# Performance work log

Measured on AMD Instinct MI355X. Metric: run time of the kernel, lower is better.

The kernel has to match this reference:

```python
import jax, jax.numpy as jnp
import numpy as np

N = 20000      # nodes per graph
E = 320000     # edges per graph (before self-loops)
G = 256        # graphs (strings) per side
VOCAB = 128    # NUMBER_EMBEDDINGS
D_IN = 128
HID = 64
H = 4
D_OUT = 128
NEG_SLOPE = 0.2  # PyG GATConv leaky_relu slope


def _gat(x, edge_index, W, att_s, att_d, bias, concat):
    """PyG GATConv: gather -> per-edge logits -> segment softmax over dst -> scatter.
    x: [N, F_in], W: [F_in, H*C], att_s/att_d: [H, C], bias: [H*C] or [C].
    Self-loops are added (PyG default add_self_loops=True)."""
    n = x.shape[0]
    h, c = att_s.shape
    loops = jnp.arange(n)
    src = jnp.concatenate([edge_index[0], loops])  # message sources j
    dst = jnp.concatenate([edge_index[1], loops])  # message targets i
    xh = (x @ W).reshape(n, h, c)                  # [N,H,C]
    a_s = jnp.einsum('nhc,hc->nh', xh, att_s)      # [N,H]
    a_d = jnp.einsum('nhc,hc->nh', xh, att_d)
    logits = jax.nn.leaky_relu(a_s[src] + a_d[dst], NEG_SLOPE)  # [E',H]
    m = jax.ops.segment_max(logits, dst, num_segments=n)
    m = jnp.where(jnp.isfinite(m), m, 0.0)
    e = jnp.exp(logits - m[dst])
    z = jax.ops.segment_sum(e, dst, num_segments=n)
    alpha = e / (z[dst] + 1e-16)                   # [E',H]
    msg = xh[src] * alpha[:, :, None]              # [E',H,C]
    out = jax.ops.segment_sum(msg, dst, num_segments=n)  # [N,H,C]
    out = out.reshape(n, h * c) if concat else out.mean(axis=1)
    return out + bias


def _encode(xi, ei, batch, emb, W1, as1, ad1, b1, lw1, lb1,
            W2, as2, ad2, b2, lw2, lb2, W3, as3, ad3, b3, lw3, lb3):
    e = emb[xi]  # [N, D_IN]
    x = jax.nn.relu(_gat(e, ei, W1, as1, ad1, b1, True) + e @ lw1 + lb1)
    x = jax.nn.relu(_gat(x, ei, W2, as2, ad2, b2, True) + x @ lw2 + lb2)
    x = _gat(x, ei, W3, as3, ad3, b3, False) + x @ lw3 + lb3  # [N, D_OUT]
    s = jax.ops.segment_sum(x, batch, num_segments=G)
    cnt = jax.ops.segment_sum(jnp.ones((x.shape[0],), x.dtype), batch, num_segments=G)
    return s / jnp.maximum(cnt, 1.0)[:, None]  # global_mean_pool -> [G, D_OUT]


def setup_inputs() -> dict:
    key = jax.random.key(0)
    ks = jax.random.split(key, 32)
    hc = H * HID  # 256
    def nrm(k, shape, scale=0.05):
        return jax.random.normal(k, shape, dtype=jnp.float32) * scale
    inp = {
        'x_l': jax.random.randint(ks[0], (N,), 0, VOCAB),
        'edge_l': jax.random.randint(ks[1], (2, E), 0, N),
        'batch_l': jnp.sort(jax.random.randint(ks[2], (N,), 0, G)),
        'x_r': jax.random.randint(ks[3], (N,), 0, VOCAB),
        'edge_r': jax.random.randint(ks[4], (2, E), 0, N),
        'batch_r': jnp.sort(jax.random.randint(ks[5], (N,), 0, G)),
        'emb': nrm(ks[6], (VOCAB, D_IN), 1.0),
        'W1': nrm(ks[7], (D_IN, hc)), 'as1': nrm(ks[8], (H, HID)), 'ad1': nrm(ks[9], (H, HID)),
        'b1': jnp.zeros((hc,), jnp.float32), 'lw1': nrm(ks[10], (D_IN, hc)), 'lb1': jnp.zeros((hc,), jnp.float32),
        'W2': nrm(ks[11], (hc, hc)), 'as2': nrm(ks[12], (H, HID)), 'ad2': nrm(ks[13], (H, HID)),
        'b2': jnp.zeros((hc,), jnp.float32), 'lw2': nrm(ks[14], (hc, hc)), 'lb2': jnp.zeros((hc,), jnp.float32),
        'W3': nrm(ks[15], (hc, H * D_OUT)), 'as3': nrm(ks[16], (H, D_OUT)), 'ad3': nrm(ks[17], (H, D_OUT)),
        'b3': jnp.zeros((D_OUT,), jnp.float32), 'lw3': nrm(ks[18], (hc, D_OUT)), 'lb3': jnp.zeros((D_OUT,), jnp.float32),
    }
    return inp


def reference(x_l, edge_l, batch_l, x_r, edge_r, batch_r, emb,
              W1, as1, ad1, b1, lw1, lb1,
              W2, as2, ad2, b2, lw2, lb2,
              W3, as3, ad3, b3, lw3, lb3):
    params = (emb, W1, as1, ad1, b1, lw1, lb1, W2, as2, ad2, b2, lw2, lb2,
              W3, as3, ad3, b3, lw3, lb3)
    out_l = _encode(x_l, edge_l, batch_l, *params)
    out_r = _encode(x_r, edge_r, batch_r, *params)
    return (out_l, out_r)
```

## Files before the change

kernel.cpp:

```cpp
#include <hip/hip_runtime.h>

#define GG 256

typedef __bf16 bf16x8 __attribute__((ext_vector_type(8)));
typedef __bf16 bf16x4 __attribute__((ext_vector_type(4)));
typedef float floatx4 __attribute__((ext_vector_type(4)));
typedef float f32x2 __attribute__((ext_vector_type(2)));

__device__ __forceinline__ float lrelu(float x) { return x > 0.f ? x : 0.2f * x; }

__device__ __forceinline__ int permM(int m) {
    int g = m >> 6, q = m & 63;
    return (g << 6) | ((q & 3) << 4) | (q >> 2);
}

__device__ __forceinline__ void wt1(const float* __restrict__ B, __bf16* __restrict__ Bt,
                                    int K, int M, int idx) {
    int k = idx / M, m = idx - k * M;
    Bt[(size_t)permM(m) * K + k] = (__bf16)B[idx];
}
__device__ __forceinline__ void wattn1(const float* __restrict__ W,
                                       const float* __restrict__ as_,
                                       const float* __restrict__ ad_,
                                       __bf16* __restrict__ dst, int K, int C, int idx) {
    int j = idx / K, k = idx - j * K;
    float v = 0.f;
    if (j < 8) {
        int h = j & 3;
        const float* att = (j < 4) ? as_ : ad_;
        int M = 4 * C;
        for (int c = 0; c < C; c++) v += W[(size_t)k * M + h * C + c] * att[h * C + c];
    }
    dst[(size_t)j * K + k] = (__bf16)v;
}

__global__ void k_wprep(const float* W1, const float* lw1, const float* as1, const float* ad1,
                        const float* W2, const float* lw2, const float* as2, const float* ad2,
                        const float* W3, const float* lw3, const float* as3, const float* ad3,
                        __bf16* B1t, __bf16* B2t, __bf16* B3t) {
    int idx = blockIdx.x * blockDim.x + threadIdx.x;
    if (idx < 32768) { wt1(W1, B1t, 128, 256, idx); return; }
    idx -= 32768;
    if (idx < 32768) { wt1(lw1, B1t + 256 * 128, 128, 256, idx); return; }
    idx -= 32768;
    if (idx < 2048) { wattn1(W1, as1, ad1, B1t + 512 * 128, 128, 64, idx); return; }
    idx -= 2048;
    if (idx < 65536) { wt1(W2, B2t, 256, 256, idx); return; }
    idx -= 65536;
    if (idx < 65536) { wt1(lw2, B2t + 256 * 256, 256, 256, idx); return; }
    idx -= 65536;
    if (idx < 4096) { wattn1(W2, as2, ad2, B2t + 512 * 256, 256, 64, idx); return; }
    idx -= 4096;
    if (idx < 131072) { wt1(W3, B3t, 256, 512, idx); return; }
    idx -= 131072;
    if (idx < 32768) { wt1(lw3, B3t + 512 * 256, 256, 128, idx); return; }
    idx -= 32768;
    if (idx < 4096) { wattn1(W3, as3, ad3, B3t + 640 * 256, 256, 128, idx); return; }
}

template <int K, bool EMB, bool LINBF>
__global__ __launch_bounds__(256) void k_gemm_all(const __bf16* __restrict__ A,
                                                  const int* __restrict__ xl,
                                                  const int* __restrict__ xr,
                                                  const float* __restrict__ emb,
                                                  const __bf16* __restrict__ Bt,
                                                  int n, int n1, int Mx, int Ml,
                                                  unsigned char* __restrict__ x8, int ldx,
                                                  float* __restrict__ linf,
                                                  __bf16* __restrict__ linb, int ldl,
                                                  const float* __restrict__ bias1,
                                                  const float* __restrict__ bias2,
                                                  float* __restrict__ a_s,
                                                  float* __restrict__ a_d) {
    constexpr int KS = K / 32;
    constexpr int LDK = K + 8;
    constexpr int LPR = K / 8;
    constexpr int NCH = 64 * LPR / 256;
    __shared__ __bf16 S[64 * LDK];
    int tid = threadIdx.x;
    int wave = tid >> 6, lane = tid & 63;
    int row0 = blockIdx.x * 64;
#pragma unroll
    for (int c = 0; c < NCH; c++) {
        int i = tid + c * 256;
        int r = i / LPR, ko = (i - r * LPR) * 8;
        int gr = row0 + r;
        bf16x8 v = {};
        if (gr < n) {
            if (EMB) {
                int xi = (gr < n1) ? xl[gr] : xr[gr - n1];
                const float4* src = (const float4*)(emb + ((size_t)xi << 7) + ko);
                float4 q0 = src[0], q1 = src[1];
                v = bf16x8{(__bf16)q0.x, (__bf16)q0.y, (__bf16)q0.z, (__bf16)q0.w,
                           (__bf16)q1.x, (__bf16)q1.y, (__bf16)q1.z, (__bf16)q1.w};
            } else {
                v = *(const bf16x8*)(A + (size_t)gr * K + ko);
            }
        }
        *(bf16x8*)&S[r * LDK + ko] = v;
    }
    __syncthreads();
    int kOff = (lane >> 4) * 8;
    int colBase = lane & 15;
    bf16x8 af[KS];
#pragma unroll
    for (int ks = 0; ks < KS; ks++)
        af[ks] = *(const bf16x8*)&S[(wave * 16 + colBase) * LDK + ks * 32 + kOff];
    int Mtot = Mx + Ml;
    int gr0 = row0 + wave * 16 + ((lane >> 4) << 2);
    int half = (Mtot / 128) * 64;
    int c0beg = blockIdx.y * half;
    int T = half / 64;
    bf16x8 regs[NCH];
#pragma unroll
    for (int c = 0; c < NCH; c++) {
        int i = tid + c * 256;
        int r = i / LPR, ko = (i - r * LPR) * 8;
        regs[c] = *(const bf16x8*)(Bt + (size_t)(c0beg + r) * K + ko);
    }
    for (int t = 0; t < T; t++) {
        __syncthreads();
#pragma unroll
        for (int c = 0; c < NCH; c++) {
            int i = tid + c * 256;
            int r = i / LPR, ko = (i - r * LPR) * 8;
            *(bf16x8*)&S[r * LDK + ko] = regs[c];
        }
        if (t + 1 < T) {
            int c0n = c0beg + (t + 1) * 64;
#pragma unroll
            for (int c = 0; c < NCH; c++) {
                int i = tid + c * 256;
                int r = i / LPR, ko = (i - r * LPR) * 8;
                regs[c] = *(const bf16x8*)(Bt + (size_t)(c0n + r) * K + ko);
            }
        }
        __syncthreads();
        floatx4 acc[4] = {};
#pragma unroll
        for (int ct = 0; ct < 4; ct++) {
#pragma unroll
            for (int ks = 0; ks < KS; ks++) {
                bf16x8 bf = *(const bf16x8*)&S[(ct * 16 + colBase) * LDK + ks * 32 + kOff];
                acc[ct] = __builtin_amdgcn_mfma_f32_16x16x32_bf16(af[ks], bf, acc[ct], 0, 0, 0);
            }
        }
        int c0 = c0beg + t * 64;
        if (c0 < Mx) {
#pragma unroll
            for (int r = 0; r < 4; r++) {
                int gr = gr0 + r;
                if (gr >= n) continue;
                int p = __builtin_amdgcn_cvt_pk_fp8_f32(acc[0][r], acc[1][r], 0, false);
                p = __builtin_amdgcn_cvt_pk_fp8_f32(acc[2][r], acc[3][r], p, true);
                *(unsigned int*)(x8 + (size_t)gr * ldx + c0 + colBase * 4) = (unsigned int)p;
            }
        } else {
            int c2 = c0 + colBase * 4 - Mx;
#pragma unroll
            for (int r = 0; r < 4; r++) {
                int gr = gr0 + r;
                if (gr >= n) continue;
                float v0 = acc[0][r] + bias1[c2 + 0];
                float v1 = acc[1][r] + bias1[c2 + 1];
                float v2 = acc[2][r] + bias1[c2 + 2];
                float v3 = acc[3][r] + bias1[c2 + 3];
                if (bias2) {
                    v0 += bias2[c2 + 0]; v1 += bias2[c2 + 1];
                    v2 += bias2[c2 + 2]; v3 += bias2[c2 + 3];
                }
                if (LINBF) {
                    bf16x4 o = {(__bf16)v0, (__bf16)v1, (__bf16)v2, (__bf16)v3};
                    *(bf16x4*)(linb + (size_t)gr * ldl + c2) = o;
                } else {
                    float4 o = {v0, v1, v2, v3};
                    *(float4*)(linf + (size_t)gr * ldl + c2) = o;
                }
            }
        }
    }
    if (blockIdx.y == 1) {
        floatx4 acc = {};
        const __bf16* bp = Bt + (size_t)(Mtot + colBase) * K + kOff;
#pragma unroll
        for (int ks = 0; ks < KS; ks++) {
            bf16x8 bf = *(const bf16x8*)(bp + ks * 32);
            acc = __builtin_amdgcn_mfma_f32_16x16x32_bf16(af[ks], bf, acc, 0, 0, 0);
        }
        if (colBase < 8) {
            float* dst = (colBase < 4) ? a_s : a_d;
            int h = colBase & 3;
#pragma unroll
            for (int r = 0; r < 4; r++) {
                int gr = gr0 + r;
                if (gr < n) dst[gr * 4 + h] = acc[r];
            }
        }
    }
}

__global__ void k_hist2(const int* __restrict__ el, const int* __restrict__ er,
                        int E, int n, int* __restrict__ deg) {
    int e = blockIdx.x * blockDim.x + threadIdx.x;
    if (e >= 2 * E) return;
    int d = (e < E) ? el[E + e] : er[E + (e - E)] + n;
    atomicAdd(&deg[d], 1);
}

__global__ __launch_bounds__(1024) void k_scan1(int* __restrict__ rp, int n,
                                                int* __restrict__ part) {
    __shared__ int wsum[16];
    int i = blockIdx.x * 1024 + threadIdx.x;
    int lane = threadIdx.x & 63, wid = threadIdx.x >> 6;
    int v = (i < n) ? rp[i] : 0;
    int inc = v;
#pragma unroll
    for (int off = 1; off < 64; off <<= 1) {
        int t = __shfl_up(inc, off, 64);
        if (lane >= off) inc += t;
    }
    if (lane == 63) wsum[wid] = inc;
    __syncthreads();
    if (wid == 0) {
        int wv = (lane < 16) ? wsum[lane] : 0;
        int winc = wv;
#pragma unroll
        for (int off = 1; off < 16; off <<= 1) {
            int t = __shfl_up(winc, off, 64);
            if (lane >= off) winc += t;
        }
        if (lane < 16) wsum[lane] = winc - wv;
        if (lane == 15) part[blockIdx.x] = winc;
    }
    __syncthreads();
    if (i < n) rp[i] = wsum[wid] + (inc - v);
}

__global__ void k_scan2(int* __restrict__ part, int nb) {
    int lane = threadIdx.x;
    int v = (lane < nb) ? part[lane] : 0;
    int inc = v;
#pragma unroll
    for (int off = 1; off < 64; off <<= 1) {
        int t = __shfl_up(inc, off, 64);
        if (lane >= off) inc += t;
    }
    if (lane < nb) part[lane] = inc - v;
}

__global__ __launch_bounds__(1024) void k_scan3(int* __restrict__ rp, int n,
                                                const int* __restrict__ part) {
    int i = blockIdx.x * 1024 + threadIdx.x;
    if (i < n) rp[i] += part[blockIdx.x];
}

__global__ void k_fill2(const int* __restrict__ el, const int* __restrict__ er,
                        int E, int n, int* __restrict__ rp, int* __restrict__ csr) {
    int e = blockIdx.x * blockDim.x + threadIdx.x;
    if (e >= 2 * E) return;
    int d, s;
    if (e < E) { s = el[e]; d = el[E + e]; }
    else       { s = er[e - E] + n; d = er[E + (e - E)] + n; }
    int pos = atomicAdd(&rp[d], 1);
    csr[pos] = s;
}

__device__ __forceinline__ void dec4(unsigned int u, float* f) {
    f32x2 a = __builtin_amdgcn_cvt_pk_f32_fp8(u, false);
    f32x2 b = __builtin_amdgcn_cvt_pk_f32_fp8(u, true);
    f[0] = a[0]; f[1] = a[1]; f[2] = b[0]; f[3] = b[1];
}

__global__ __launch_bounds__(256) void k_agg12(const int* __restrict__ rp,
                                               const int* __restrict__ csr,
                                               const float* __restrict__ a_s,
                                               const float* __restrict__ a_d,
                                               const unsigned char* __restrict__ x8,
                                               const __bf16* __restrict__ lin,
                                               __bf16* __restrict__ out_bf, int n) {
    int wv = (int)((blockIdx.x * blockDim.x + threadIdx.x) >> 6);
    int lane = threadIdx.x & 63;
    int sub = lane >> 5, sl = lane & 31;
    int node = wv * 2 + sub;
    if (node >= n) return;
    int c0 = sl * 8;
    int h = sl >> 3;
    int start = node ? rp[node - 1] : 0;
    int end = rp[node];
    float ad = a_d[node * 4 + h];
    float z = __expf(lrelu(a_s[node * 4 + h] + ad));
    float acc[8];
    {
        uint2 u = *(const uint2*)(x8 + (size_t)node * 256 + c0);
        float f[8];
        dec4(u.x, f); dec4(u.y, f + 4);
#pragma unroll
        for (int j = 0; j < 8; j++) acc[j] = z * f[j];
    }
    uint2 u0 = {}, u1 = {}, u2 = {};
    float A0 = 0.f, A1 = 0.f, A2 = 0.f;
    if (start < end) {
        int s = csr[start];
        u0 = *(const uint2*)(x8 + (size_t)s * 256 + c0);
        A0 = a_s[s * 4 + h];
    }
    if (start + 1 < end) {
        int s = csr[start + 1];
        u1 = *(const uint2*)(x8 + (size_t)s * 256 + c0);
        A1 = a_s[s * 4 + h];
    }
    if (start + 2 < end) {
        int s = csr[start + 2];
        u2 = *(const uint2*)(x8 + (size_t)s * 256 + c0);
        A2 = a_s[s * 4 + h];
    }
    for (int e = start; e < end; e++) {
        uint2 uc = u0;
        float ac = A0;
        u0 = u1; A0 = A1;
        u1 = u2; A1 = A2;
        if (e + 3 < end) {
            int s = csr[e + 3];
            u2 = *(const uint2*)(x8 + (size_t)s * 256 + c0);
            A2 = a_s[s * 4 + h];
        }
        float w = __expf(lrelu(ac + ad));
        z += w;
        float f[8];
        dec4(uc.x, f); dec4(uc.y, f + 4);
#pragma unroll
        for (int q = 0; q < 8; q++) acc[q] += w * f[q];
    }
    float inv = 1.f / (z + 1e-16f);
    bf16x8 l = *(const bf16x8*)(lin + (size_t)node * 256 + c0);
    bf16x8 r;
#pragma unroll
    for (int j = 0; j < 8; j++)
        r[j] = (__bf16)fmaxf(acc[j] * inv + (float)l[j], 0.f);
    *(bf16x8*)(out_bf + (size_t)node * 256 + c0) = r;
}

__global__ __launch_bounds__(256) void k_agg3(const int* __restrict__ rp,
                                              const int* __restrict__ csr,
                                              const float* __restrict__ a_s,
                                              const float* __restrict__ a_d,
                                              const unsigned int* __restrict__ x8,
                                              float* __restrict__ mean, int n) {
    int wv = (int)((blockIdx.x * blockDim.x + threadIdx.x) >> 6);
    int lane = threadIdx.x & 63;
    int sub = lane >> 5, sl = lane & 31;
    int node = wv * 2 + sub;
    if (node >= n) return;
    int h = sl >> 3;
    int start = node ? rp[node - 1] : 0;
    int end = rp[node];
    float ad = a_d[node * 4 + h];
    float z = __expf(lrelu(a_s[node * 4 + h] + ad));
    float acc[16];
    {
        uint4 u = *(const uint4*)(x8 + (size_t)node * 128 + sl * 4);
        float f[16];
        dec4(u.x, f); dec4(u.y, f + 4); dec4(u.z, f + 8); dec4(u.w, f + 12);
#pragma unroll
        for (int j = 0; j < 16; j++) acc[j] = z * f[j];
    }
    uint4 u0 = {}, u1 = {}, u2 = {};
    float A0 = 0.f, A1 = 0.f, A2 = 0.f;
    if (start < end) {
        int s = csr[start];
        u0 = *(const uint4*)(x8 + (size_t)s * 128 + sl * 4);
        A0 = a_s[s * 4 + h];
    }
    if (start + 1 < end) {
        int s = csr[start + 1];
        u1 = *(const uint4*)(x8 + (size_t)s * 128 + sl * 4);
        A1 = a_s[s * 4 + h];
    }
    if (start + 2 < end) {
        int s = csr[start + 2];
        u2 = *(const uint4*)(x8 + (size_t)s * 128 + sl * 4);
        A2 = a_s[s * 4 + h];
    }
    for (int e = start; e < end; e++) {
        uint4 uc = u0;
        float ac = A0;
        u0 = u1; A0 = A1;
        u1 = u2; A1 = A2;
        if (e + 3 < end) {
            int s = csr[e + 3];
            u2 = *(const uint4*)(x8 + (size_t)s * 128 + sl * 4);
            A2 = a_s[s * 4 + h];
        }
        float w = __expf(lrelu(ac + ad));
        z += w;
        float f[16];
        dec4(uc.x, f); dec4(uc.y, f + 4); dec4(uc.z, f + 8); dec4(uc.w, f + 12);
#pragma unroll
        for (int q = 0; q < 16; q++) acc[q] += w * f[q];
    }
    float scale = 0.25f / (z + 1e-16f);
#pragma unroll
    for (int j = 0; j < 16; j++) {
        float v = acc[j] * scale;
        v += __shfl_xor(v, 8, 64);
        v += __shfl_xor(v, 16, 64);
        acc[j] = v;
    }
    if ((sl & 24) == 0) {
        float4* op = (float4*)(mean + (size_t)node * 128 + sl * 16);
#pragma unroll
        for (int q = 0; q < 4; q++) {
            float4 o = {acc[4 * q], acc[4 * q + 1], acc[4 * q + 2], acc[4 * q + 3]};
            op[q] = o;
        }
    }
}

__global__ __launch_bounds__(128) void k_pool(const float* __restrict__ mean,
                                              const float* __restrict__ lin3,
                                              const float* __restrict__ b3,
                                              const int* __restrict__ bl,
                                              const int* __restrict__ br,
                                              int n, float* __restrict__ out) {
    int g = blockIdx.x, c = threadIdx.x;
    const int* b = (g < GG) ? bl : br;
    int tg = (g < GG) ? g : g - GG;
    int off = (g < GG) ? 0 : n;
    int s, e;
    { int lo = 0, hi = n; while (lo < hi) { int m = (lo + hi) >> 1; if (b[m] < tg) lo = m + 1; else hi = m; } s = lo; }
    { int lo = 0, hi = n; while (lo < hi) { int m = (lo + hi) >> 1; if (b[m] < tg + 1) lo = m + 1; else hi = m; } e = lo; }
    s += off; e += off;
    float acc = 0.f;
    for (int i = s; i < e; i++)
        acc += mean[(size_t)i * 128 + c] + lin3[(size_t)i * 128 + c];
    int cnt = e - s;
    out[(size_t)g * 128 + c] = cnt > 0 ? acc / (float)cnt + b3[c] : 0.f;
}

static inline int cdiv(int a, int b) { return (a + b - 1) / b; }

extern "C" void kernel_launch(void* const* d_in, const int* in_sizes, int n_in,
                              void* d_out, int out_size, void* d_ws, size_t ws_size,
                              hipStream_t stream) {
    const int* x_l = (const int*)d_in[0];
    const int* edge_l = (const int*)d_in[1];
    const int* batch_l = (const int*)d_in[2];
    const int* x_r = (const int*)d_in[3];
    const int* edge_r = (const int*)d_in[4];
    const int* batch_r = (const int*)d_in[5];
    const float* emb = (const float*)d_in[6];
    const float* W1 = (const float*)d_in[7];
    const float* as1 = (const float*)d_in[8];
    const float* ad1 = (const float*)d_in[9];
    const float* b1 = (const float*)d_in[10];
    const float* lw1 = (const float*)d_in[11];
    const float* lb1 = (const float*)d_in[12];
    const float* W2 = (const float*)d_in[13];
    const float* as2 = (const float*)d_in[14];
    const float* ad2 = (const float*)d_in[15];
    const float* b2 = (const float*)d_in[16];
    const float* lw2 = (const float*)d_in[17];
    const float* lb2 = (const float*)d_in[18];
    const float* W3 = (const float*)d_in[19];
    const float* as3 = (const float*)d_in[20];
    const float* ad3 = (const float*)d_in[21];
    const float* b3 = (const float*)d_in[22];
    const float* lw3 = (const float*)d_in[23];
    const float* lb3 = (const float*)d_in[24];

    const int n = in_sizes[0];
    const int E = in_sizes[1] / 2;
    const int N2 = 2 * n;
    const int NB = cdiv(N2, 1024);

    float* MEAN = (float*)d_ws;
    float* L3 = MEAN + (size_t)N2 * 128;
    float* a_s = L3 + (size_t)N2 * 128;
    float* a_d = a_s + (size_t)N2 * 4;
    int* rp = (int*)(a_d + (size_t)N2 * 4);
    int* csr = rp + N2;
    int* part = csr + 2 * E;
    __bf16* LINb = (__bf16*)(part + 64);
    unsigned char* X8a = (unsigned char*)(LINb + (size_t)N2 * 256);
    unsigned char* X8b = X8a + (size_t)N2 * 256;
    __bf16* Abf = (__bf16*)(X8b + (size_t)N2 * 512);
    __bf16* B1t = Abf + (size_t)N2 * 256;
    __bf16* B2t = B1t + 528 * 128;
    __bf16* B3t = B2t + 528 * 256;

    const int TB = 256;
    dim3 blk(TB);

    k_wprep<<<cdiv(370688, TB), blk, 0, stream>>>(W1, lw1, as1, ad1, W2, lw2, as2, ad2,
                                                  W3, lw3, as3, ad3, B1t, B2t, B3t);

    hipMemsetAsync(rp, 0, sizeof(int) * (size_t)N2, stream);
    k_hist2<<<cdiv(2 * E, TB), blk, 0, stream>>>(edge_l, edge_r, E, n, rp);
    k_scan1<<<NB, 1024, 0, stream>>>(rp, N2, part);
    k_scan2<<<1, 64, 0, stream>>>(part, NB);
    k_scan3<<<NB, 1024, 0, stream>>>(rp, N2, part);
    k_fill2<<<cdiv(2 * E, TB), blk, 0, stream>>>(edge_l, edge_r, E, n, rp, csr);

    k_gemm_all<128, true, true><<<dim3(cdiv(N2, 64), 2), blk, 0, stream>>>(
        nullptr, x_l, x_r, emb, B1t, N2, n, 256, 256, X8a, 256, nullptr, LINb, 256, lb1, b1, a_s, a_d);
    k_agg12<<<cdiv(N2, 8), blk, 0, stream>>>(rp, csr, a_s, a_d, X8a, LINb, Abf, N2);

    k_gemm_all<256, false, true><<<dim3(cdiv(N2, 64), 2), blk, 0, stream>>>(
        Abf, nullptr, nullptr, nullptr, B2t, N2, n, 256, 256, X8a, 256, nullptr, LINb, 256, lb2, b2, a_s, a_d);
    k_agg12<<<cdiv(N2, 8), blk, 0, stream>>>(rp, csr, a_s, a_d, X8a, LINb, Abf, N2);

    k_gemm_all<256, false, false><<<dim3(cdiv(N2, 64), 2), blk, 0, stream>>>(
        Abf, nullptr, nullptr, nullptr, B3t, N2, n, 512, 128, X8b, 512, L3, nullptr, 128, lb3, nullptr, a_s, a_d);
    k_agg3<<<cdiv(N2, 8), blk, 0, stream>>>(rp, csr, a_s, a_d, (const unsigned int*)X8b, MEAN, N2);
    k_pool<<<2 * GG, 128, 0, stream>>>(MEAN, L3, b3, batch_l, batch_r, n, (float*)d_out);
}
```

Measured before the change: 450.7 us.

## Map one node per wavefront in aggregation kernels and swizzle block order

The aggregation kernels now give each node a full 64-lane wavefront instead of half a wavefront, so every lane handles fewer channels per edge (4 fp8 bytes in layers 1-2, 8 in layer 3). Accumulation uses packed f32x2 math, and the layer-3 head-mean reduction changes to shuffles across lanes 16 and 32. A block-index swizzle interleaves blocks from the two graph halves, likely to spread L2/XCD locality. The intent is more memory-level parallelism for the gathers, at the cost of twice as many waves, narrower loads per lane and more redundant per-edge index and logit work.

```diff
diff --git a/kernel.cpp b/kernel.cpp
--- a/kernel.cpp
+++ b/kernel.cpp
@@ -55,7 +55,7 @@
     idx -= 131072;
     if (idx < 32768) { wt1(lw3, B3t + 512 * 256, 256, 128, idx); return; }
     idx -= 32768;
-    if (idx < 4096) { wattn1(W3, as3, ad3, B3t + 640 * 256, 256, 128, idx); return; }
+    if (idx < 4096) { wattn1(W3, as3, ad3, B3t + 640 * 256, 256, 128, idx); }
 }
 
 template <int K, bool EMB, bool LINBF>
@@ -265,10 +265,12 @@
     csr[pos] = s;
 }
 
-__device__ __forceinline__ void dec4(unsigned int u, float* f) {
-    f32x2 a = __builtin_amdgcn_cvt_pk_f32_fp8(u, false);
-    f32x2 b = __builtin_amdgcn_cvt_pk_f32_fp8(u, true);
-    f[0] = a[0]; f[1] = a[1]; f[2] = b[0]; f[3] = b[1];
+__device__ __forceinline__ int swz_block(int bid, int nbx) {
+    if (nbx & 7) return bid;
+    int halfb = nbx >> 1;
+    int grp = bid >> 3, r = bid & 7;
+    int j = grp * 4 + (r & 3);
+    return (r < 4) ? j : halfb + j;
 }
 
 __global__ __launch_bounds__(256) void k_agg12(const int* __restrict__ rp,
@@ -278,40 +280,110 @@
                                                const unsigned char* __restrict__ x8,
                                                const __bf16* __restrict__ lin,
                                                __bf16* __restrict__ out_bf, int n) {
-    int wv = (int)((blockIdx.x * blockDim.x + threadIdx.x) >> 6);
+    int nb = swz_block(blockIdx.x, gridDim.x);
     int lane = threadIdx.x & 63;
-    int sub = lane >> 5, sl = lane & 31;
-    int node = wv * 2 + sub;
+    int node = nb * 4 + (threadIdx.x >> 6);
     if (node >= n) return;
-    int c0 = sl * 8;
-    int h = sl >> 3;
+    int c0 = lane * 4;
+    int h = lane >> 4;
     int start = node ? rp[node - 1] : 0;
     int end = rp[node];
     float ad = a_d[node * 4 + h];
     float z = __expf(lrelu(a_s[node * 4 + h] + ad));
-    float acc[8];
+    f32x2 acc0, acc1;
     {
-        uint2 u = *(const uint2*)(x8 + (size_t)node * 256 + c0);
-        float f[8];
-        dec4(u.x, f); dec4(u.y, f + 4);
-#pragma unroll
-        for (int j = 0; j < 8; j++) acc[j] = z * f[j];
+        unsigned int u = *(const unsigned int*)(x8 + (size_t)node * 256 + c0);
+        f32x2 lo = __builtin_amdgcn_cvt_pk_f32_fp8(u, false);
+        f32x2 hi = __builtin_amdgcn_cvt_pk_f32_fp8(u, true);
+        f32x2 zz = {z, z};
+        acc0 = zz * lo;
+        acc1 = zz * hi;
+    }
+    unsigned int u0 = 0, u1 = 0, u2 = 0;
+    float A0 = 0.f, A1 = 0.f, A2 = 0.f;
+    if (start < end) {
+        int s = csr[start];
+        u0 = *(const unsigned int*)(x8 + (size_t)s * 256 + c0);
+        A0 = a_s[s * 4 + h];
+    }
+    if (start + 1 < end) {
+        int s = csr[start + 1];
+        u1 = *(const unsigned int*)(x8 + (size_t)s * 256 + c0);
+        A1 = a_s[s * 4 + h];
+    }
+    if (start + 2 < end) {
+        int s = csr[start + 2];
+        u2 = *(const unsigned int*)(x8 + (size_t)s * 256 + c0);
+        A2 = a_s[s * 4 + h];
+    }
+    for (int e = start; e < end; e++) {
+        unsigned int uc = u0;
+        float ac = A0;
+        u0 = u1; A0 = A1;
+        u1 = u2; A1 = A2;
+        if (e + 3 < end) {
+            int s = csr[e + 3];
+            u2 = *(const unsigned int*)(x8 + (size_t)s * 256 + c0);
+            A2 = a_s[s * 4 + h];
+        }
+        float w = __expf(lrelu(ac + ad));
+        z += w;
+        f32x2 lo = __builtin_amdgcn_cvt_pk_f32_fp8(uc, false);
+        f32x2 hi = __builtin_amdgcn_cvt_pk_f32_fp8(uc, true);
+        f32x2 wv = {w, w};
+        acc0 += wv * lo;
+        acc1 += wv * hi;
+    }
+    float inv = 1.f / (z + 1e-16f);
+    bf16x4 l = *(const bf16x4*)(lin + (size_t)node * 256 + c0);
+    bf16x4 r;
+    r[0] = (__bf16)fmaxf(acc0[0] * inv + (float)l[0], 0.f);
+    r[1] = (__bf16)fmaxf(acc0[1] * inv + (float)l[1], 0.f);
+    r[2] = (__bf16)fmaxf(acc1[0] * inv + (float)l[2], 0.f);
+    r[3] = (__bf16)fmaxf(acc1[1] * inv + (float)l[3], 0.f);
+    *(bf16x4*)(out_bf + (size_t)node * 256 + c0) = r;
+}
+
+__global__ __launch_bounds__(256) void k_agg3(const int* __restrict__ rp,
+                                              const int* __restrict__ csr,
+                                              const float* __restrict__ a_s,
+                                              const float* __restrict__ a_d,
+                                              const unsigned int* __restrict__ x8,
+                                              float* __restrict__ mean, int n) {
+    int nb = swz_block(blockIdx.x, gridDim.x);
+    int lane = threadIdx.x & 63;
+    int node = nb * 4 + (threadIdx.x >> 6);
+    if (node >= n) return;
+    int h = lane >> 4;
+    int dw = lane * 2;
+    int start = node ? rp[node - 1] : 0;
+    int end = rp[node];
+    float ad = a_d[node * 4 + h];
+    float z = __expf(lrelu(a_s[node * 4 + h] + ad));
+    f32x2 acc[4];
+    {
+        uint2 u = *(const uint2*)(x8 + (size_t)node * 128 + dw);
+        f32x2 zz = {z, z};
+        acc[0] = zz * __builtin_amdgcn_cvt_pk_f32_fp8(u.x, false);
+        acc[1] = zz * __builtin_amdgcn_cvt_pk_f32_fp8(u.x, true);
+        acc[2] = zz * __builtin_amdgcn_cvt_pk_f32_fp8(u.y, false);
+        acc[3] = zz * __builtin_amdgcn_cvt_pk_f32_fp8(u.y, true);
     }
     uint2 u0 = {}, u1 = {}, u2 = {};
     float A0 = 0.f, A1 = 0.f, A2 = 0.f;
     if (start < end) {
         int s = csr[start];
-        u0 = *(const uint2*)(x8 + (size_t)s * 256 + c0);
+        u0 = *(const uint2*)(x8 + (size_t)s * 128 + dw);
         A0 = a_s[s * 4 + h];
     }
     if (start + 1 < end) {
         int s = csr[start + 1];
-        u1 = *(const uint2*)(x8 + (size_t)s * 256 + c0);
+        u1 = *(const uint2*)(x8 + (size_t)s * 128 + dw);
         A1 = a_s[s * 4 + h];
     }
     if (start + 2 < end) {
         int s = csr[start + 2];
-        u2 = *(const uint2*)(x8 + (size_t)s * 256 + c0);
+        u2 = *(const uint2*)(x8 + (size_t)s * 128 + dw);
         A2 = a_s[s * 4 + h];
     }
     for (int e = start; e < end; e++) {
@@ -321,98 +393,32 @@
         u1 = u2; A1 = A2;
         if (e + 3 < end) {
             int s = csr[e + 3];
-            u2 = *(const uint2*)(x8 + (size_t)s * 256 + c0);
+            u2 = *(const uint2*)(x8 + (size_t)s * 128 + dw);
             A2 = a_s[s * 4 + h];
         }
         float w = __expf(lrelu(ac + ad));
         z += w;
-        float f[8];
-        dec4(uc.x, f); dec4(uc.y, f + 4);
-#pragma unroll
-        for (int q = 0; q < 8; q++) acc[q] += w * f[q];
-    }
-    float inv = 1.f / (z + 1e-16f);
-    bf16x8 l = *(const bf16x8*)(lin + (size_t)node * 256 + c0);
-    bf16x8 r;
-#pragma unroll
-    for (int j = 0; j < 8; j++)
-        r[j] = (__bf16)fmaxf(acc[j] * inv + (float)l[j], 0.f);
-    *(bf16x8*)(out_bf + (size_t)node * 256 + c0) = r;
-}
-
-__global__ __launch_bounds__(256) void k_agg3(const int* __restrict__ rp,
-                                              const int* __restrict__ csr,
-                                              const float* __restrict__ a_s,
-                                              const float* __restrict__ a_d,
-                                              const unsigned int* __restrict__ x8,
-                                              float* __restrict__ mean, int n) {
-    int wv = (int)((blockIdx.x * blockDim.x + threadIdx.x) >> 6);
-    int lane = threadIdx.x & 63;
-    int sub = lane >> 5, sl = lane & 31;
-    int node = wv * 2 + sub;
-    if (node >= n) return;
-    int h = sl >> 3;
-    int start = node ? rp[node - 1] : 0;
-    int end = rp[node];
-    float ad = a_d[node * 4 + h];
-    float z = __expf(lrelu(a_s[node * 4 + h] + ad));
-    float acc[16];
-    {
-        uint4 u = *(const uint4*)(x8 + (size_t)node * 128 + sl * 4);
-        float f[16];
-        dec4(u.x, f); dec4(u.y, f + 4); dec4(u.z, f + 8); dec4(u.w, f + 12);
-#pragma unroll
-        for (int j = 0; j < 16; j++) acc[j] = z * f[j];
-    }
-    uint4 u0 = {}, u1 = {}, u2 = {};
-    float A0 = 0.f, A1 = 0.f, A2 = 0.f;
-    if (start < end) {
-        int s = csr[start];
-        u0 = *(const uint4*)(x8 + (size_t)s * 128 + sl * 4);
-        A0 = a_s[s * 4 + h];
-    }
-    if (start + 1 < end) {
-        int s = csr[start + 1];
-        u1 = *(const uint4*)(x8 + (size_t)s * 128 + sl * 4);
-        A1 = a_s[s * 4 + h];
-    }
-    if (start + 2 < end) {
-        int s = csr[start + 2];
-        u2 = *(const uint4*)(x8 + (size_t)s * 128 + sl * 4);
-        A2 = a_s[s * 4 + h];
-    }
-    for (int e = start; e < end; e++) {
-        uint4 uc = u0;
-        float ac = A0;
-        u0 = u1; A0 = A1;
-        u1 = u2; A1 = A2;
-        if (e + 3 < end) {
-            int s = csr[e + 3];
-            u2 = *(const uint4*)(x8 + (size_t)s * 128 + sl * 4);
-            A2 = a_s[s * 4 + h];
-        }
-        float w = __expf(lrelu(ac + ad));
-        z += w;
-        float f[16];
-        dec4(uc.x, f); dec4(uc.y, f + 4); dec4(uc.z, f + 8); dec4(uc.w, f + 12);
-#pragma unroll
-        for (int q = 0; q < 16; q++) acc[q] += w * f[q];
+        f32x2 wv = {w, w};
+        acc[0] += wv * __builtin_amdgcn_cvt_pk_f32_fp8(uc.x, false);
+        acc[1] += wv * __builtin_amdgcn_cvt_pk_f32_fp8(uc.x, true);
+        acc[2] += wv * __builtin_amdgcn_cvt_pk_f32_fp8(uc.y, false);
+        acc[3] += wv * __builtin_amdgcn_cvt_pk_f32_fp8(uc.y, true);
     }
     float scale = 0.25f / (z + 1e-16f);
-#pragma unroll
-    for (int j = 0; j < 16; j++) {
-        float v = acc[j] * scale;
-        v += __shfl_xor(v, 8, 64);
-        v += __shfl_xor(v, 16, 64);
-        acc[j] = v;
-    }
-    if ((sl & 24) == 0) {
-        float4* op = (float4*)(mean + (size_t)node * 128 + sl * 16);
-#pragma unroll
-        for (int q = 0; q < 4; q++) {
-            float4 o = {acc[4 * q], acc[4 * q + 1], acc[4 * q + 2], acc[4 * q + 3]};
-            op[q] = o;
-        }
+    float v[8];
+#pragma unroll
+    for (int j = 0; j < 8; j++) {
+        float t = acc[j >> 1][j & 1] * scale;
+        t += __shfl_xor(t, 16, 64);
+        t += __shfl_xor(t, 32, 64);
+        v[j] = t;
+    }
+    if (lane < 16) {
+        float4* op = (float4*)(mean + (size_t)node * 128 + lane * 8);
+        float4 o0 = {v[0], v[1], v[2], v[3]};
+        float4 o1 = {v[4], v[5], v[6], v[7]};
+        op[0] = o0;
+        op[1] = o1;
     }
 }
 
@@ -503,14 +509,14 @@
 
     k_gemm_all<128, true, true><<<dim3(cdiv(N2, 64), 2), blk, 0, stream>>>(
         nullptr, x_l, x_r, emb, B1t, N2, n, 256, 256, X8a, 256, nullptr, LINb, 256, lb1, b1, a_s, a_d);
-    k_agg12<<<cdiv(N2, 8), blk, 0, stream>>>(rp, csr, a_s, a_d, X8a, LINb, Abf, N2);
+    k_agg12<<<cdiv(N2, 4), blk, 0, stream>>>(rp, csr, a_s, a_d, X8a, LINb, Abf, N2);
 
     k_gemm_all<256, false, true><<<dim3(cdiv(N2, 64), 2), blk, 0, stream>>>(
         Abf, nullptr, nullptr, nullptr, B2t, N2, n, 256, 256, X8a, 256, nullptr, LINb, 256, lb2, b2, a_s, a_d);
-    k_agg12<<<cdiv(N2, 8), blk, 0, stream>>>(rp, csr, a_s, a_d, X8a, LINb, Abf, N2);
+    k_agg12<<<cdiv(N2, 4), blk, 0, stream>>>(rp, csr, a_s, a_d, X8a, LINb, Abf, N2);
 
     k_gemm_all<256, false, false><<<dim3(cdiv(N2, 64), 2), blk, 0, stream>>>(
         Abf, nullptr, nullptr, nullptr, B3t, N2, n, 512, 128, X8b, 512, L3, nullptr, 128, lb3, nullptr, a_s, a_d);
-    k_agg3<<<cdiv(N2, 8), blk, 0, stream>>>(rp, csr, a_s, a_d, (const unsigned int*)X8b, MEAN, N2);
+    k_agg3<<<cdiv(N2, 4), blk, 0, stream>>>(rp, csr, a_s, a_d, (const unsigned int*)X8b, MEAN, N2);
     k_pool<<<2 * GG, 128, 0, stream>>>(MEAN, L3, b3, batch_l, batch_r, n, (float*)d_out);
 }
```

Result: slower. 512.1 us (+13.6%).

## Split each node's edge list across wave halves and swizzle aggregation blocks

Applied to the files above, without the earlier changes.

The aggregation kernels now assign one full wave per destination node instead of two nodes per wave. The two 32-lane halves process alternating edges and are combined with a cross-half shuffle, which doubles the memory-level parallelism per node and halves the serial edge loop. The prefetch is made unconditional by clamping to the last edge, and a block-index swizzle interleaves blocks from the left and right graphs, presumably to spread memory traffic. The cost is twice as many waves and extra shuffle reductions.

```diff
diff --git a/kernel.cpp b/kernel.cpp
--- a/kernel.cpp
+++ b/kernel.cpp
@@ -55,7 +55,7 @@
     idx -= 131072;
     if (idx < 32768) { wt1(lw3, B3t + 512 * 256, 256, 128, idx); return; }
     idx -= 32768;
-    if (idx < 4096) { wattn1(W3, as3, ad3, B3t + 640 * 256, 256, 128, idx); return; }
+    if (idx < 4096) { wattn1(W3, as3, ad3, B3t + 640 * 256, 256, 128, idx); }
 }
 
 template <int K, bool EMB, bool LINBF>
@@ -271,6 +271,14 @@
     f[0] = a[0]; f[1] = a[1]; f[2] = b[0]; f[3] = b[1];
 }
 
+__device__ __forceinline__ int swz_block(int bid, int nbx) {
+    if (nbx & 7) return bid;
+    int halfb = nbx >> 1;
+    int grp = bid >> 3, r = bid & 7;
+    int j = grp * 4 + (r & 3);
+    return (r < 4) ? j : halfb + j;
+}
+
 __global__ __launch_bounds__(256) void k_agg12(const int* __restrict__ rp,
                                                const int* __restrict__ csr,
                                                const float* __restrict__ a_s,
@@ -278,19 +286,20 @@
                                                const unsigned char* __restrict__ x8,
                                                const __bf16* __restrict__ lin,
                                                __bf16* __restrict__ out_bf, int n) {
-    int wv = (int)((blockIdx.x * blockDim.x + threadIdx.x) >> 6);
+    int nb = swz_block(blockIdx.x, gridDim.x);
     int lane = threadIdx.x & 63;
-    int sub = lane >> 5, sl = lane & 31;
-    int node = wv * 2 + sub;
+    int half = lane >> 5, sl = lane & 31;
+    int node = nb * 4 + (threadIdx.x >> 6);
     if (node >= n) return;
     int c0 = sl * 8;
     int h = sl >> 3;
     int start = node ? rp[node - 1] : 0;
     int end = rp[node];
     float ad = a_d[node * 4 + h];
-    float z = __expf(lrelu(a_s[node * 4 + h] + ad));
-    float acc[8];
-    {
+    float z = 0.f;
+    float acc[8] = {};
+    if (half == 0) {
+        z = __expf(lrelu(a_s[node * 4 + h] + ad));
         uint2 u = *(const uint2*)(x8 + (size_t)node * 256 + c0);
         float f[8];
         dec4(u.x, f); dec4(u.y, f + 4);
@@ -299,31 +308,32 @@
     }
     uint2 u0 = {}, u1 = {}, u2 = {};
     float A0 = 0.f, A1 = 0.f, A2 = 0.f;
-    if (start < end) {
-        int s = csr[start];
+    int e0 = start + half;
+    if (e0 < end) {
+        int s = csr[e0];
         u0 = *(const uint2*)(x8 + (size_t)s * 256 + c0);
         A0 = a_s[s * 4 + h];
     }
-    if (start + 1 < end) {
-        int s = csr[start + 1];
+    if (e0 + 2 < end) {
+        int s = csr[e0 + 2];
         u1 = *(const uint2*)(x8 + (size_t)s * 256 + c0);
         A1 = a_s[s * 4 + h];
     }
-    if (start + 2 < end) {
-        int s = csr[start + 2];
+    if (e0 + 4 < end) {
+        int s = csr[e0 + 4];
         u2 = *(const uint2*)(x8 + (size_t)s * 256 + c0);
         A2 = a_s[s * 4 + h];
     }
-    for (int e = start; e < end; e++) {
+    for (int e = e0; e < end; e += 2) {
         uint2 uc = u0;
         float ac = A0;
         u0 = u1; A0 = A1;
         u1 = u2; A1 = A2;
-        if (e + 3 < end) {
-            int s = csr[e + 3];
-            u2 = *(const uint2*)(x8 + (size_t)s * 256 + c0);
-            A2 = a_s[s * 4 + h];
-        }
+        int pn = e + 6;
+        pn = pn < end ? pn : end - 1;
+        int s = csr[pn];
+        u2 = *(const uint2*)(x8 + (size_t)s * 256 + c0);
+        A2 = a_s[s * 4 + h];
         float w = __expf(lrelu(ac + ad));
         z += w;
         float f[8];
@@ -331,13 +341,18 @@
 #pragma unroll
         for (int q = 0; q < 8; q++) acc[q] += w * f[q];
     }
-    float inv = 1.f / (z + 1e-16f);
-    bf16x8 l = *(const bf16x8*)(lin + (size_t)node * 256 + c0);
-    bf16x8 r;
-#pragma unroll
-    for (int j = 0; j < 8; j++)
-        r[j] = (__bf16)fmaxf(acc[j] * inv + (float)l[j], 0.f);
-    *(bf16x8*)(out_bf + (size_t)node * 256 + c0) = r;
+    z += __shfl_xor(z, 32, 64);
+#pragma unroll
+    for (int j = 0; j < 8; j++) acc[j] += __shfl_xor(acc[j], 32, 64);
+    if (half == 0) {
+        float inv = 1.f / (z + 1e-16f);
+        bf16x8 l = *(const bf16x8*)(lin + (size_t)node * 256 + c0);
+        bf16x8 r;
+#pragma unroll
+        for (int j = 0; j < 8; j++)
+            r[j] = (__bf16)fmaxf(acc[j] * inv + (float)l[j], 0.f);
+        *(bf16x8*)(out_bf + (size_t)node * 256 + c0) = r;
+    }
 }
 
 __global__ __launch_bounds__(256) void k_agg3(const int* __restrict__ rp,
@@ -346,18 +361,19 @@
                                               const float* __restrict__ a_d,
                                               const unsigned int* __restrict__ x8,
                                               float* __restrict__ mean, int n) {
-    int wv = (int)((blockIdx.x * blockDim.x + threadIdx.x) >> 6);
+    int nb = swz_block(blockIdx.x, gridDim.x);
     int lane = threadIdx.x & 63;
-    int sub = lane >> 5, sl = lane & 31;
-    int node = wv * 2 + sub;
+    int half = lane >> 5, sl = lane & 31;
+    int node = nb * 4 + (threadIdx.x >> 6);
     if (node >= n) return;
     int h = sl >> 3;
     int start = node ? rp[node - 1] : 0;
     int end = rp[node];
     float ad = a_d[node * 4 + h];
-    float z = __expf(lrelu(a_s[node * 4 + h] + ad));
-    float acc[16];
-    {
+    float z = 0.f;
+    float acc[16] = {};
+    if (half == 0) {
+        z = __expf(lrelu(a_s[node * 4 + h] + ad));
         uint4 u = *(const uint4*)(x8 + (size_t)node * 128 + sl * 4);
         float f[16];
         dec4(u.x, f); dec4(u.y, f + 4); dec4(u.z, f + 8); dec4(u.w, f + 12);
@@ -366,31 +382,32 @@
     }
     uint4 u0 = {}, u1 = {}, u2 = {};
     float A0 = 0.f, A1 = 0.f, A2 = 0.f;
-    if (start < end) {
-        int s = csr[start];
+    int e0 = start + half;
+    if (e0 < end) {
+        int s = csr[e0];
         u0 = *(const uint4*)(x8 + (size_t)s * 128 + sl * 4);
         A0 = a_s[s * 4 + h];
     }
-    if (start + 1 < end) {
-        int s = csr[start + 1];
+    if (e0 + 2 < end) {
+        int s = csr[e0 + 2];
         u1 = *(const uint4*)(x8 + (size_t)s * 128 + sl * 4);
         A1 = a_s[s * 4 + h];
     }
-    if (start + 2 < end) {
-        int s = csr[start + 2];
+    if (e0 + 4 < end) {
+        int s = csr[e0 + 4];
         u2 = *(const uint4*)(x8 + (size_t)s * 128 + sl * 4);
         A2 = a_s[s * 4 + h];
     }
-    for (int e = start; e < end; e++) {
+    for (int e = e0; e < end; e += 2) {
         uint4 uc = u0;
         float ac = A0;
         u0 = u1; A0 = A1;
         u1 = u2; A1 = A2;
-        if (e + 3 < end) {
-            int s = csr[e + 3];
-            u2 = *(const uint4*)(x8 + (size_t)s * 128 + sl * 4);
-            A2 = a_s[s * 4 + h];
-        }
+        int pn = e + 6;
+        pn = pn < end ? pn : end - 1;
+        int s = csr[pn];
+        u2 = *(const uint4*)(x8 + (size_t)s * 128 + sl * 4);
+        A2 = a_s[s * 4 + h];
         float w = __expf(lrelu(ac + ad));
         z += w;
         float f[16];
@@ -398,6 +415,9 @@
 #pragma unroll
         for (int q = 0; q < 16; q++) acc[q] += w * f[q];
     }
+    z += __shfl_xor(z, 32, 64);
+#pragma unroll
+    for (int j = 0; j < 16; j++) acc[j] += __shfl_xor(acc[j], 32, 64);
     float scale = 0.25f / (z + 1e-16f);
 #pragma unroll
     for (int j = 0; j < 16; j++) {
@@ -406,8 +426,8 @@
         v += __shfl_xor(v, 16, 64);
         acc[j] = v;
     }
-    if ((sl & 24) == 0) {
-        float4* op = (float4*)(mean + (size_t)node * 128 + sl * 16);
+    if (lane < 8) {
+        float4* op = (float4*)(mean + (size_t)node * 128 + lane * 16);
 #pragma unroll
         for (int q = 0; q < 4; q++) {
             float4 o = {acc[4 * q], acc[4 * q + 1], acc[4 * q + 2], acc[4 * q + 3]};
@@ -503,14 +523,14 @@
 
     k_gemm_all<128, true, true><<<dim3(cdiv(N2, 64), 2), blk, 0, stream>>>(
         nullptr, x_l, x_r, emb, B1t, N2, n, 256, 256, X8a, 256, nullptr, LINb, 256, lb1, b1, a_s, a_d);
-    k_agg12<<<cdiv(N2, 8), blk, 0, stream>>>(rp, csr, a_s, a_d, X8a, LINb, Abf, N2);
+    k_agg12<<<cdiv(N2, 4), blk, 0, stream>>>(rp, csr, a_s, a_d, X8a, LINb, Abf, N2);
 
     k_gemm_all<256, false, true><<<dim3(cdiv(N2, 64), 2), blk, 0, stream>>>(
         Abf, nullptr, nullptr, nullptr, B2t, N2, n, 256, 256, X8a, 256, nullptr, LINb, 256, lb2, b2, a_s, a_d);
-    k_agg12<<<cdiv(N2, 8), blk, 0, stream>>>(rp, csr, a_s, a_d, X8a, LINb, Abf, N2);
+    k_agg12<<<cdiv(N2, 4), blk, 0, stream>>>(rp, csr, a_s, a_d, X8a, LINb, Abf, N2);
 
     k_gemm_all<256, false, false><<<dim3(cdiv(N2, 64), 2), blk, 0, stream>>>(
         Abf, nullptr, nullptr, nullptr, B3t, N2, n, 512, 128, X8b, 512, L3, nullptr, 128, lb3, nullptr, a_s, a_d);
-    k_agg3<<<cdiv(N2, 8), blk, 0, stream>>>(rp, csr, a_s, a_d, (const unsigned int*)X8b, MEAN, N2);
+    k_agg3<<<cdiv(N2, 4), blk, 0, stream>>>(rp, csr, a_s, a_d, (const unsigned int*)X8b, MEAN, N2);
     k_pool<<<2 * GG, 128, 0, stream>>>(MEAN, L3, b3, batch_l, batch_r, n, (float*)d_out);
 }
```

New measurement: 447.5 us. No clear change (-0.7%).
